# Kernel tuning notes

Measured on AMD Instinct MI355X. Metric: run time of the kernel, lower is better.

Reference implementation:

```python
import jax, jax.numpy as jnp
import numpy as np

IN_SIZE = 2048 + 1  # features + scalar reward, per RolloutEncoder.__init__
HIDDEN = 1024       # config['rollout_enc_size']
T = 8192            # rollout buffer length


def setup_inputs() -> dict:
    key = jax.random.key(0)
    k1, k2, k3, k4, k5, k6 = jax.random.split(key, 6)
    s = 1.0 / np.sqrt(HIDDEN)  # torch GRUCell init scale
    return {
        "features": jax.random.normal(k1, (T, 2048), dtype=jnp.float32),
        "rewards": jax.random.normal(k2, (T,), dtype=jnp.float32),
        "w_ih": jax.random.uniform(k3, (3 * HIDDEN, IN_SIZE), jnp.float32, -s, s),
        "w_hh": jax.random.uniform(k4, (3 * HIDDEN, HIDDEN), jnp.float32, -s, s),
        "b_ih": jax.random.uniform(k5, (3 * HIDDEN,), jnp.float32, -s, s),
        "b_hh": jax.random.uniform(k6, (3 * HIDDEN,), jnp.float32, -s, s),
    }


def reference(features, rewards, w_ih, w_hh, b_ih, b_hh):
    H = w_hh.shape[1]
    # concat features with reward -> [T, 2049], matching torch.cat((features, reward.unsqueeze(0)), dim=1)
    x = jnp.concatenate([features, rewards[:, None]], axis=1)
    # precompute all input-side gate pre-activations in one big GEMM: [T, 3H]
    gi = x @ w_ih.T + b_ih
    gi_r, gi_z, gi_n = jnp.split(gi, 3, axis=1)

    w_hr, w_hz, w_hn = jnp.split(w_hh, 3, axis=0)
    b_hr, b_hz, b_hn = jnp.split(b_hh, 3)

    def step(h, g):  # h: [H]
        gr, gz, gn = g
        r = jax.nn.sigmoid(gr + h @ w_hr.T + b_hr)
        z = jax.nn.sigmoid(gz + h @ w_hz.T + b_hz)
        n = jnp.tanh(gn + r * (h @ w_hn.T + b_hn))
        h_new = (1.0 - z) * n + z * h
        return h_new, None

    h0 = jnp.zeros((H,), dtype=features.dtype)
    # dream_buffer.pop() consumes the LAST transition first -> reverse scan
    h_final, _ = jax.lax.scan(step, h0, (gi_r, gi_z, gi_n), reverse=True)
    return h_final[None, :]  # [1, H] like torch hidden
```

## Files before the change

### kernel.cpp

```cpp
#include <hip/hip_runtime.h>
#include <hip/hip_bf16.h>
#include <stdint.h>

#define T_STEPS 8192
#define HID     1024
#define IN_F    2048
#define N3H     3072
#define NREP    8

__global__ void init_pairs(unsigned int* pairs) {
    int i = blockIdx.x * blockDim.x + threadIdx.x;
    if (i < 2 * NREP * HID) pairs[i] = 0u;
}

__device__ __forceinline__ uint4 load_x4_scoped(const unsigned int* p) {
    uint4 r;
    asm volatile("global_load_dwordx4 %0, %1, off sc0 sc1\n\t"
                 "s_waitcnt vmcnt(0)"
                 : "=v"(r) : "v"(p) : "memory");
    return r;
}
__device__ __forceinline__ void store_scoped(unsigned int* p, unsigned int v) {
    asm volatile("global_store_dword %0, %1, off sc0 sc1"
                 :: "v"(p), "v"(v) : "memory");
}

#define GBM 64
#define GBN 64
#define GBK 32

__global__ __launch_bounds__(256) void gi_gemm(
    const float* __restrict__ feat,
    const float* __restrict__ rew,
    const float* __restrict__ w_ih,
    const float* __restrict__ b_ih,
    float* __restrict__ gi)
{
    __shared__ float As[GBK][GBM + 4];
    __shared__ float Bs[GBK][GBN + 4];

    const int tid = threadIdx.x;
    const int n0 = blockIdx.x * GBN;
    const int t0 = blockIdx.y * GBM;
    const int tx = tid & 15, ty = tid >> 4;
    const int lr = tid >> 3;
    const int lc = (tid & 7) * 4;

    float acc[4][4] = {{0.f}};

    for (int k0 = 0; k0 < IN_F; k0 += GBK) {
#pragma unroll
        for (int hh = 0; hh < 2; hh++) {
            const int r = lr + 32 * hh;
            const float4 a = *(const float4*)(feat + (size_t)(t0 + r) * IN_F + k0 + lc);
            As[lc + 0][r] = a.x; As[lc + 1][r] = a.y;
            As[lc + 2][r] = a.z; As[lc + 3][r] = a.w;
            const float* brow = w_ih + (size_t)(n0 + r) * (IN_F + 1) + k0 + lc;
            Bs[lc + 0][r] = brow[0]; Bs[lc + 1][r] = brow[1];
            Bs[lc + 2][r] = brow[2]; Bs[lc + 3][r] = brow[3];
        }
        __syncthreads();
#pragma unroll
        for (int kk = 0; kk < GBK; kk++) {
            const float4 a = *(const float4*)&As[kk][ty * 4];
            const float4 b = *(const float4*)&Bs[kk][tx * 4];
            acc[0][0] += a.x * b.x; acc[0][1] += a.x * b.y; acc[0][2] += a.x * b.z; acc[0][3] += a.x * b.w;
            acc[1][0] += a.y * b.x; acc[1][1] += a.y * b.y; acc[1][2] += a.y * b.z; acc[1][3] += a.y * b.w;
            acc[2][0] += a.z * b.x; acc[2][1] += a.z * b.y; acc[2][2] += a.z * b.z; acc[2][3] += a.z * b.w;
            acc[3][0] += a.w * b.x; acc[3][1] += a.w * b.y; acc[3][2] += a.w * b.z; acc[3][3] += a.w * b.w;
        }
        __syncthreads();
    }

    const int m = t0 + ty * 4;
    const int n = n0 + tx * 4;
    float wlast[4], bi[4];
#pragma unroll
    for (int c = 0; c < 4; c++) {
        wlast[c] = w_ih[(size_t)(n + c) * (IN_F + 1) + IN_F];
        bi[c]    = b_ih[n + c];
    }
#pragma unroll
    for (int r = 0; r < 4; r++) {
        const float rwv = rew[m + r];
        float4 v;
        v.x = acc[r][0] + rwv * wlast[0] + bi[0];
        v.y = acc[r][1] + rwv * wlast[1] + bi[1];
        v.z = acc[r][2] + rwv * wlast[2] + bi[2];
        v.w = acc[r][3] + rwv * wlast[3] + bi[3];
        *(float4*)(gi + (size_t)(m + r) * N3H + n) = v;
    }
}

__global__ __launch_bounds__(256, 2) void gru_scan(
    const float* __restrict__ gi,
    const float* __restrict__ w_hh,
    const float* __restrict__ b_hh,
    unsigned int* pairs,
    float* __restrict__ out)
{
    __shared__ float4 w_lds[3][4][HID / 4];
    __shared__ float4 h_lds[HID / 4];

    const int tid  = threadIdx.x;
    const int g    = blockIdx.x;
    const int j0   = g * 4;
    const int wave = tid >> 6;
    const int lane = tid & 63;
    const int myj  = j0 + wave;
    const int rep  = g & (NREP - 1);

#pragma unroll
    for (int r = 0; r < 12; r++) {
        const int gate = r >> 2, jl = r & 3;
        const float4* src = (const float4*)(w_hh + (size_t)(gate * HID + j0 + jl) * HID);
        w_lds[gate][jl][tid] = src[tid];
    }
    float b_r = 0.f, b_z = 0.f, b_n = 0.f;
    if (lane == 0) {
        b_r = b_hh[myj];
        b_z = b_hh[HID + myj];
        b_n = b_hh[2 * HID + myj];
    }
    __syncthreads();

    float* h_f = (float*)h_lds;

    for (int i = 0; i < T_STEPS; i++) {
        const int t = T_STEPS - 1 - i;
        unsigned int* rbuf  = pairs + ((size_t)(i & 1) * NREP + rep) * HID;
        unsigned int* sbase = pairs + (size_t)((i + 1) & 1) * NREP * HID + myj;

        float gi_r = 0.f, gi_z = 0.f, gi_n = 0.f;
        if (lane == 0) {
            const float* girow = gi + (size_t)t * N3H;
            gi_r = girow[myj];
            gi_z = girow[HID + myj];
            gi_n = girow[2 * HID + myj];
        }

        {
            const unsigned int want = (unsigned int)(i & 3);
            uint4 v;
            for (;;) {
                v = load_x4_scoped(rbuf + tid * 4);
                if (((v.x & 3u) == want) && ((v.y & 3u) == want) &&
                    ((v.z & 3u) == want) && ((v.w & 3u) == want))
                    break;
                __builtin_amdgcn_s_sleep(1);
            }
            float4 hv;
            hv.x = __uint_as_float(v.x);
            hv.y = __uint_as_float(v.y);
            hv.z = __uint_as_float(v.z);
            hv.w = __uint_as_float(v.w);
            h_lds[tid] = hv;
        }
        __syncthreads();

        float ar = 0.f, az = 0.f, an = 0.f;
        const float4* wr = w_lds[0][wave];
        const float4* wz = w_lds[1][wave];
        const float4* wn = w_lds[2][wave];
#pragma unroll
        for (int m4 = 0; m4 < 4; m4++) {
            const int idx = lane + 64 * m4;
            const float4 h4 = h_lds[idx];
            const float4 r4 = wr[idx];
            const float4 z4 = wz[idx];
            const float4 n4 = wn[idx];
            ar += h4.x * r4.x + h4.y * r4.y + h4.z * r4.z + h4.w * r4.w;
            az += h4.x * z4.x + h4.y * z4.y + h4.z * z4.z + h4.w * z4.w;
            an += h4.x * n4.x + h4.y * n4.y + h4.z * n4.z + h4.w * n4.w;
        }
#pragma unroll
        for (int off = 32; off > 0; off >>= 1) {
            ar += __shfl_down(ar, off);
            az += __shfl_down(az, off);
            an += __shfl_down(an, off);
        }

        if (lane == 0) {
            const float hjold = h_f[myj];
            const float r = 1.f / (1.f + __expf(-(gi_r + ar + b_r)));
            const float z = 1.f / (1.f + __expf(-(gi_z + az + b_z)));
            const float n = tanhf(gi_n + r * (an + b_n));
            const float hnew = (1.f - z) * n + z * hjold;
            if (i == T_STEPS - 1) {
                out[myj] = hnew;
            } else {
                const unsigned int pk =
                    (__float_as_uint(hnew) & ~3u) | (unsigned int)((i + 1) & 3);
#pragma unroll
                for (int rr = 0; rr < NREP; rr++)
                    store_scoped(sbase + rr * HID, pk);
            }
        }
        __syncthreads();
    }
}

extern "C" void kernel_launch(void* const* d_in, const int* in_sizes, int n_in,
                              void* d_out, int out_size, void* d_ws, size_t ws_size,
                              hipStream_t stream) {
    const float* feat = (const float*)d_in[0];
    const float* rew  = (const float*)d_in[1];
    const float* w_ih = (const float*)d_in[2];
    const float* w_hh = (const float*)d_in[3];
    const float* b_ih = (const float*)d_in[4];
    const float* b_hh = (const float*)d_in[5];
    float* out = (float*)d_out;

    float* gi = (float*)d_ws;
    unsigned int* pairs =
        (unsigned int*)((char*)d_ws + (size_t)T_STEPS * N3H * sizeof(float));

    hipLaunchKernelGGL(init_pairs, dim3((2 * NREP * HID + 255) / 256), dim3(256), 0, stream, pairs);
    hipLaunchKernelGGL(gi_gemm, dim3(N3H / GBN, T_STEPS / GBM), dim3(256), 0, stream,
                       feat, rew, w_ih, b_ih, gi);
    hipLaunchKernelGGL(gru_scan, dim3(256), dim3(256), 0, stream,
                       gi, w_hh, b_hh, pairs, out);
}
```

Measured before the change: 18.47 ms.

## Double-buffer h in LDS, DPP wave reductions, parallel replica stores, drop trailing barrier

The GRU scan now double-buffers the hidden state in LDS, which removes the second __syncthreads per step. Shuffle-based reductions are replaced by DPP row operations plus a readlane broadcast. All lanes now compute the gate math, and each of the first NREP lanes stores one replica in parallel instead of lane 0 looping over them. The replica count also rises from 8 to 16 to spread polling across more buffers, at the cost of extra store traffic per step.

```diff
diff --git a/kernel.cpp b/kernel.cpp
--- a/kernel.cpp
+++ b/kernel.cpp
@@ -6,7 +6,7 @@
 #define HID     1024
 #define IN_F    2048
 #define N3H     3072
-#define NREP    8
+#define NREP    16
 
 __global__ void init_pairs(unsigned int* pairs) {
     int i = blockIdx.x * blockDim.x + threadIdx.x;
@@ -92,6 +92,26 @@
     }
 }
 
+__device__ __forceinline__ float wave_red_sum(float x) {
+    int v;
+    v = __builtin_amdgcn_update_dpp(0, __float_as_int(x), 0x111, 0xf, 0xf, true);
+    x += __int_as_float(v);
+    v = __builtin_amdgcn_update_dpp(0, __float_as_int(x), 0x112, 0xf, 0xf, true);
+    x += __int_as_float(v);
+    v = __builtin_amdgcn_update_dpp(0, __float_as_int(x), 0x114, 0xf, 0xf, true);
+    x += __int_as_float(v);
+    v = __builtin_amdgcn_update_dpp(0, __float_as_int(x), 0x118, 0xf, 0xf, true);
+    x += __int_as_float(v);
+    v = __builtin_amdgcn_update_dpp(0, __float_as_int(x), 0x142, 0xf, 0xf, true);
+    x += __int_as_float(v);
+    v = __builtin_amdgcn_update_dpp(0, __float_as_int(x), 0x143, 0xf, 0xf, true);
+    x += __int_as_float(v);
+    return x;
+}
+__device__ __forceinline__ float bcast_lane(float x, int lane) {
+    return __int_as_float(__builtin_amdgcn_readlane(__float_as_int(x), lane));
+}
+
 __global__ __launch_bounds__(256, 2) void gru_scan(
     const float* __restrict__ gi,
     const float* __restrict__ w_hh,
@@ -100,7 +120,7 @@
     float* __restrict__ out)
 {
     __shared__ float4 w_lds[3][4][HID / 4];
-    __shared__ float4 h_lds[HID / 4];
+    __shared__ float4 h_lds[2][HID / 4];
 
     const int tid  = threadIdx.x;
     const int g    = blockIdx.x;
@@ -116,37 +136,32 @@
         const float4* src = (const float4*)(w_hh + (size_t)(gate * HID + j0 + jl) * HID);
         w_lds[gate][jl][tid] = src[tid];
     }
-    float b_r = 0.f, b_z = 0.f, b_n = 0.f;
-    if (lane == 0) {
-        b_r = b_hh[myj];
-        b_z = b_hh[HID + myj];
-        b_n = b_hh[2 * HID + myj];
-    }
+    const float b_r = b_hh[myj];
+    const float b_z = b_hh[HID + myj];
+    const float b_n = b_hh[2 * HID + myj];
     __syncthreads();
 
-    float* h_f = (float*)h_lds;
+    const float4* const wr = w_lds[0][wave];
+    const float4* const wz = w_lds[1][wave];
+    const float4* const wn = w_lds[2][wave];
 
     for (int i = 0; i < T_STEPS; i++) {
         const int t = T_STEPS - 1 - i;
-        unsigned int* rbuf  = pairs + ((size_t)(i & 1) * NREP + rep) * HID;
-        unsigned int* sbase = pairs + (size_t)((i + 1) & 1) * NREP * HID + myj;
-
-        float gi_r = 0.f, gi_z = 0.f, gi_n = 0.f;
-        if (lane == 0) {
-            const float* girow = gi + (size_t)t * N3H;
-            gi_r = girow[myj];
-            gi_z = girow[HID + myj];
-            gi_n = girow[2 * HID + myj];
-        }
+        const unsigned int* rbuf = pairs + ((size_t)(i & 1) * NREP + rep) * HID;
+
+        const float* girow = gi + (size_t)t * N3H;
+        const float gi_r = girow[myj];
+        const float gi_z = girow[HID + myj];
+        const float gi_n = girow[2 * HID + myj];
 
         {
             const unsigned int want = (unsigned int)(i & 3);
             uint4 v;
             for (;;) {
                 v = load_x4_scoped(rbuf + tid * 4);
-                if (((v.x & 3u) == want) && ((v.y & 3u) == want) &&
-                    ((v.z & 3u) == want) && ((v.w & 3u) == want))
-                    break;
+                const unsigned int m = (v.x ^ want) | (v.y ^ want) |
+                                       (v.z ^ want) | (v.w ^ want);
+                if ((m & 3u) == 0u) break;
                 __builtin_amdgcn_s_sleep(1);
             }
             float4 hv;
@@ -154,18 +169,16 @@
             hv.y = __uint_as_float(v.y);
             hv.z = __uint_as_float(v.z);
             hv.w = __uint_as_float(v.w);
-            h_lds[tid] = hv;
+            h_lds[i & 1][tid] = hv;
         }
         __syncthreads();
 
+        const float4* hb = h_lds[i & 1];
         float ar = 0.f, az = 0.f, an = 0.f;
-        const float4* wr = w_lds[0][wave];
-        const float4* wz = w_lds[1][wave];
-        const float4* wn = w_lds[2][wave];
 #pragma unroll
         for (int m4 = 0; m4 < 4; m4++) {
             const int idx = lane + 64 * m4;
-            const float4 h4 = h_lds[idx];
+            const float4 h4 = hb[idx];
             const float4 r4 = wr[idx];
             const float4 z4 = wz[idx];
             const float4 n4 = wn[idx];
@@ -173,30 +186,26 @@
             az += h4.x * z4.x + h4.y * z4.y + h4.z * z4.z + h4.w * z4.w;
             an += h4.x * n4.x + h4.y * n4.y + h4.z * n4.z + h4.w * n4.w;
         }
-#pragma unroll
-        for (int off = 32; off > 0; off >>= 1) {
-            ar += __shfl_down(ar, off);
-            az += __shfl_down(az, off);
-            an += __shfl_down(an, off);
-        }
-
-        if (lane == 0) {
-            const float hjold = h_f[myj];
-            const float r = 1.f / (1.f + __expf(-(gi_r + ar + b_r)));
-            const float z = 1.f / (1.f + __expf(-(gi_z + az + b_z)));
-            const float n = tanhf(gi_n + r * (an + b_n));
-            const float hnew = (1.f - z) * n + z * hjold;
-            if (i == T_STEPS - 1) {
-                out[myj] = hnew;
-            } else {
-                const unsigned int pk =
-                    (__float_as_uint(hnew) & ~3u) | (unsigned int)((i + 1) & 3);
-#pragma unroll
-                for (int rr = 0; rr < NREP; rr++)
-                    store_scoped(sbase + rr * HID, pk);
-            }
-        }
-        __syncthreads();
+
+        const float sr = bcast_lane(wave_red_sum(ar), 63);
+        const float sz = bcast_lane(wave_red_sum(az), 63);
+        const float sn = bcast_lane(wave_red_sum(an), 63);
+
+        const float hold = ((const float*)hb)[myj];
+
+        const float r = 1.f / (1.f + __expf(-(gi_r + sr + b_r)));
+        const float z = 1.f / (1.f + __expf(-(gi_z + sz + b_z)));
+        const float n = tanhf(gi_n + r * (sn + b_n));
+        const float hnew = (1.f - z) * n + z * hold;
+
+        if (i == T_STEPS - 1) {
+            if (lane == 0) out[myj] = hnew;
+        } else if (lane < NREP) {
+            const unsigned int pk =
+                (__float_as_uint(hnew) & ~3u) | (unsigned int)((i + 1) & 3);
+            unsigned int* nbuf = pairs + (size_t)((i + 1) & 1) * NREP * HID;
+            store_scoped(nbuf + lane * HID + myj, pk);
+        }
     }
 }
 
```

Result: slower. 25.74 ms (+39.4%).
